# Kernel tuning notes

Hardware: AMD Instinct MI355X
Metric: run time of the kernel (lower is better)

## Reference

```python
import jax, jax.numpy as jnp
import numpy as np

B, S, QD, KD, AD, H = 64, 2048, 1024, 512, 512, 8
NEG = -1e10  # masked_fill value from original code
SCALING = 1.0  # default forward arg


def setup_inputs() -> dict:
    key = jax.random.key(0)
    ks = jax.random.split(key, 6)
    query = jax.random.normal(ks[0], (B, QD), dtype=jnp.float32)
    keys = jax.random.normal(ks[1], (B, S, KD), dtype=jnp.float32)
    value = jax.random.normal(ks[2], (B, S, KD), dtype=jnp.float32)
    key_len = jax.random.randint(ks[3], (B,), 1, S + 1, dtype=jnp.int32)
    Wq = jax.random.normal(ks[4], (H, AD, QD), dtype=jnp.float32) * 0.02
    Wk = jax.random.normal(ks[5], (H, AD, KD), dtype=jnp.float32) * 0.02
    return {"query": query, "keys": keys, "value": value, "key_len": key_len,
            "Wq": Wq, "Wk": Wk}


def reference(query, keys, value, key_len, Wq, Wk):
    # per-head query projection: (B, H, AD)
    q = jnp.einsum('bq,haq->bha', query, Wq)
    # per-head key projection: (B, H, S, AD)
    k = jnp.einsum('bsk,hak->bhsa', keys, Wk)
    # single-step dot attention energies: (B, H, S)
    energy = jnp.einsum('bha,bhsa->bhs', q, k)
    # padding mask: positions >= key_len are masked
    mask = jnp.arange(keys.shape[1])[None, None, :] >= key_len[:, None, None]
    energy = jnp.where(mask, NEG, energy)
    attn = jax.nn.softmax(energy * SCALING, axis=-1)  # (B, H, S)
    # per-head contexts: (B, H, KD), concatenated over heads -> (B, H*KD)
    context = jnp.einsum('bhs,bsd->bhd', attn, value)
    contexts = context.reshape(context.shape[0], -1)
    return contexts, attn
```

## Files before the change

### kernel.cpp

```cpp
#include <hip/hip_runtime.h>
#include <math.h>


#define B_  64
#define S_  2048
#define QD_ 1024
#define KD_ 512
#define AD_ 512
#define H_  8

__global__ __launch_bounds__(256) void k1_qproj(const float* __restrict__ query,
                                                const float* __restrict__ Wq,
                                                float* __restrict__ qo) {
    __shared__ float As[16][65];
    __shared__ float Ws[64][65];
    const int t = threadIdx.x;
    const int m0 = blockIdx.x * 16, n0 = blockIdx.y * 64;
    const int nl = t & 63, mb = (t >> 6) * 4;
    float acc[4] = {0.f, 0.f, 0.f, 0.f};
    for (int kc = 0; kc < QD_; kc += 64) {
#pragma unroll
        for (int i = 0; i < 4; ++i) {
            int idx = t + i * 256, r = idx >> 6, c = idx & 63;
            As[r][c] = query[(m0 + r) * QD_ + kc + c];
        }
#pragma unroll
        for (int i = 0; i < 16; ++i) {
            int idx = t + i * 256, r = idx >> 6, c = idx & 63;
            Ws[r][c] = Wq[(size_t)(n0 + r) * QD_ + kc + c];
        }
        __syncthreads();
#pragma unroll
        for (int k = 0; k < 64; ++k) {
            float w = Ws[nl][k];
#pragma unroll
            for (int j = 0; j < 4; ++j) acc[j] += As[mb + j][k] * w;
        }
        __syncthreads();
    }
#pragma unroll
    for (int j = 0; j < 4; ++j)
        qo[(m0 + mb + j) * (H_ * AD_) + n0 + nl] = acc[j];
}

__global__ __launch_bounds__(256) void k2_qk(const float* __restrict__ q,
                                             const float* __restrict__ Wk,
                                             float* __restrict__ qk) {
    __shared__ float As[16][65];
    __shared__ float Ws[64][65];
    const int t = threadIdx.x;
    const int m0 = blockIdx.x * 16, n0 = blockIdx.y * 64, h = blockIdx.z;
    const float* Wh = Wk + (size_t)h * AD_ * KD_;
    const int nl = t & 63, mb = (t >> 6) * 4;
    float acc[4] = {0.f, 0.f, 0.f, 0.f};
    for (int ac = 0; ac < AD_; ac += 64) {
#pragma unroll
        for (int i = 0; i < 4; ++i) {
            int idx = t + i * 256, r = idx >> 6, c = idx & 63;
            As[r][c] = q[(m0 + r) * (H_ * AD_) + h * AD_ + ac + c];
        }
#pragma unroll
        for (int i = 0; i < 16; ++i) {
            int idx = t + i * 256, r = idx >> 6, c = idx & 63;
            Ws[r][c] = Wh[(size_t)(ac + r) * KD_ + n0 + c];
        }
        __syncthreads();
#pragma unroll
        for (int k = 0; k < 64; ++k) {
            float w = Ws[k][nl];
#pragma unroll
            for (int j = 0; j < 4; ++j) acc[j] += As[mb + j][k] * w;
        }
        __syncthreads();
    }
#pragma unroll
    for (int j = 0; j < 4; ++j)
        qk[(m0 + mb + j) * (H_ * KD_) + h * KD_ + n0 + nl] = acc[j];
}

__global__ __launch_bounds__(256) void k3_energy(const float* __restrict__ keys,
                                                 const float* __restrict__ qk,
                                                 const int* __restrict__ key_len,
                                                 float* __restrict__ energy) {
    const int b = blockIdx.y;
    const int klen = key_len[b];
    const int s0 = blockIdx.x * 128;
    if (s0 >= klen) return;
    const int t = threadIdx.x;
    const int lane = t & 63, w = t >> 6;

    const float4* qk4 = reinterpret_cast<const float4*>(qk + (size_t)b * (H_ * KD_));
    float qkr[8][8];
#pragma unroll
    for (int h = 0; h < H_; ++h) {
        float4 u0 = qk4[h * (KD_ / 4) + lane * 2];
        float4 u1 = qk4[h * (KD_ / 4) + lane * 2 + 1];
        qkr[h][0] = u0.x; qkr[h][1] = u0.y; qkr[h][2] = u0.z; qkr[h][3] = u0.w;
        qkr[h][4] = u1.x; qkr[h][5] = u1.y; qkr[h][6] = u1.z; qkr[h][7] = u1.w;
    }

    const int sbeg = s0 + w * 32;
    for (int i = 0; i < 32; ++i) {
        int s = sbeg + i;
        if (s >= klen) break;
        const float4* kp = reinterpret_cast<const float4*>(
            keys + (size_t)(b * S_ + s) * KD_ + lane * 8);
        float4 k0 = kp[0], k1 = kp[1];
        float kf[8] = {k0.x, k0.y, k0.z, k0.w, k1.x, k1.y, k1.z, k1.w};
        float partial[8];
#pragma unroll
        for (int h = 0; h < H_; ++h) {
            float p = 0.f;
#pragma unroll
            for (int j = 0; j < 8; ++j) p += kf[j] * qkr[h][j];
            partial[h] = p;
        }
#pragma unroll
        for (int h = 0; h < H_; ++h) {
#pragma unroll
            for (int off = 32; off >= 1; off >>= 1)
                partial[h] += __shfl_xor(partial[h], off, 64);
        }
#pragma unroll
        for (int h = 0; h < H_; ++h)
            if (lane == h) energy[((size_t)b * H_ + h) * S_ + s] = partial[h];
    }
}

__global__ __launch_bounds__(256) void k4_softmax(const float* __restrict__ energy,
                                                  const int* __restrict__ key_len,
                                                  float* __restrict__ attn,
                                                  float* __restrict__ ctx_zero) {
    const int bh = blockIdx.x;
    const int b = bh >> 3;
    const int t = threadIdx.x;
    ctx_zero[bh * 512 + t] = 0.f;
    ctx_zero[bh * 512 + 256 + t] = 0.f;

    const int klen = key_len[b];
    const float* e = energy + (size_t)bh * S_;
    float ev[8];
    float m = -3.0e38f;
#pragma unroll
    for (int j = 0; j < 8; ++j) {
        int s = t + j * 256;
        float x = (s < klen) ? e[s] : -3.0e38f;
        ev[j] = x;
        m = fmaxf(m, x);
    }
#pragma unroll
    for (int off = 32; off >= 1; off >>= 1) m = fmaxf(m, __shfl_xor(m, off, 64));
    __shared__ float redm[4];
    if ((t & 63) == 0) redm[t >> 6] = m;
    __syncthreads();
    m = fmaxf(fmaxf(redm[0], redm[1]), fmaxf(redm[2], redm[3]));

    float sum = 0.f;
#pragma unroll
    for (int j = 0; j < 8; ++j) {
        int s = t + j * 256;
        float p = (s < klen) ? __expf(ev[j] - m) : 0.f;
        ev[j] = p;
        sum += p;
    }
#pragma unroll
    for (int off = 32; off >= 1; off >>= 1) sum += __shfl_xor(sum, off, 64);
    __shared__ float reds[4];
    if ((t & 63) == 0) reds[t >> 6] = sum;
    __syncthreads();
    sum = reds[0] + reds[1] + reds[2] + reds[3];
    const float inv = 1.f / sum;

    float* a = attn + (size_t)bh * S_;
#pragma unroll
    for (int j = 0; j < 8; ++j) a[t + j * 256] = ev[j] * inv;
}

__global__ __launch_bounds__(256) void k5_context(const float* __restrict__ value,
                                                  const float* __restrict__ attn,
                                                  const int* __restrict__ key_len,
                                                  float* __restrict__ ctx) {
    const int b = blockIdx.y;
    const int klen = key_len[b];
    const int s_base = blockIdx.x * 128;
    if (s_base >= klen) return;
    const int t = threadIdx.x;

    __shared__ float at[8][128];
#pragma unroll
    for (int i = 0; i < 4; ++i) {
        int idx = t + i * 256, h = idx >> 7, si = idx & 127;
        int s = s_base + si;
        at[h][si] = (s < klen) ? attn[((size_t)b * H_ + h) * S_ + s] : 0.f;
    }
    __syncthreads();

    const int tt = t & 127;
    const int sh = t >> 7;
    const int d = tt * 4;
    const int siBeg = sh * 64;
    const int siEnd = min(siBeg + 64, klen - s_base);

    float4 acc[8];
#pragma unroll
    for (int h = 0; h < H_; ++h) acc[h] = make_float4(0.f, 0.f, 0.f, 0.f);

    for (int si = siBeg; si < siEnd; ++si) {
        const float4 v = *reinterpret_cast<const float4*>(
            value + (size_t)(b * S_ + s_base + si) * KD_ + d);
#pragma unroll
        for (int h = 0; h < H_; ++h) {
            float a = at[h][si];
            acc[h].x += a * v.x; acc[h].y += a * v.y;
            acc[h].z += a * v.z; acc[h].w += a * v.w;
        }
    }

    float* cb = ctx + (size_t)b * (H_ * KD_);
#pragma unroll
    for (int h = 0; h < H_; ++h) {
        atomicAdd(&cb[h * KD_ + d + 0], acc[h].x);
        atomicAdd(&cb[h * KD_ + d + 1], acc[h].y);
        atomicAdd(&cb[h * KD_ + d + 2], acc[h].z);
        atomicAdd(&cb[h * KD_ + d + 3], acc[h].w);
    }
}

extern "C" void kernel_launch(void* const* d_in, const int* in_sizes, int n_in,
                              void* d_out, int out_size, void* d_ws, size_t ws_size,
                              hipStream_t stream) {
    const float* query   = (const float*)d_in[0];
    const float* keys    = (const float*)d_in[1];
    const float* value   = (const float*)d_in[2];
    const int*   key_len = (const int*)d_in[3];
    const float* Wq      = (const float*)d_in[4];
    const float* Wk      = (const float*)d_in[5];

    float* out = (float*)d_out;
    float* ctx_out  = out;
    float* attn_out = out + (size_t)B_ * H_ * KD_;

    float* ws    = (float*)d_ws;
    float* q_ws  = ws;
    float* qk_ws = ws + (size_t)B_ * H_ * AD_;
    float* e_ws  = qk_ws + (size_t)B_ * H_ * KD_;

    hipLaunchKernelGGL(k1_qproj, dim3(4, 64), dim3(256), 0, stream, query, Wq, q_ws);
    hipLaunchKernelGGL(k2_qk, dim3(4, 8, 8), dim3(256), 0, stream, q_ws, Wk, qk_ws);
    hipLaunchKernelGGL(k3_energy, dim3(16, 64), dim3(256), 0, stream,
                       keys, qk_ws, key_len, e_ws);
    hipLaunchKernelGGL(k4_softmax, dim3(512), dim3(256), 0, stream,
                       e_ws, key_len, attn_out, ctx_out);
    hipLaunchKernelGGL(k5_context, dim3(16, 64), dim3(256), 0, stream,
                       value, attn_out, key_len, ctx_out);
}
```

Before: 645.2 us.

## Halve energy block size, use transpose-style shuffle reduction, replace context atomics with partial reduce

```diff
diff --git a/kernel.cpp b/kernel.cpp
--- a/kernel.cpp
+++ b/kernel.cpp
@@ -84,7 +84,7 @@
                                                  float* __restrict__ energy) {
     const int b = blockIdx.y;
     const int klen = key_len[b];
-    const int s0 = blockIdx.x * 128;
+    const int s0 = blockIdx.x * 64;
     if (s0 >= klen) return;
     const int t = threadIdx.x;
     const int lane = t & 63, w = t >> 6;
@@ -99,43 +99,63 @@
         qkr[h][4] = u1.x; qkr[h][5] = u1.y; qkr[h][6] = u1.z; qkr[h][7] = u1.w;
     }
 
-    const int sbeg = s0 + w * 32;
-    for (int i = 0; i < 32; ++i) {
-        int s = sbeg + i;
-        if (s >= klen) break;
+    const int sbeg = s0 + w * 16;
+    const int count = min(16, klen - sbeg);
+    if (count <= 0) return;
+
+    auto row = [&](int s) {
         const float4* kp = reinterpret_cast<const float4*>(
             keys + (size_t)(b * S_ + s) * KD_ + lane * 8);
         float4 k0 = kp[0], k1 = kp[1];
         float kf[8] = {k0.x, k0.y, k0.z, k0.w, k1.x, k1.y, k1.z, k1.w};
-        float partial[8];
-#pragma unroll
-        for (int h = 0; h < H_; ++h) {
-            float p = 0.f;
-#pragma unroll
-            for (int j = 0; j < 8; ++j) p += kf[j] * qkr[h][j];
-            partial[h] = p;
-        }
-#pragma unroll
-        for (int h = 0; h < H_; ++h) {
-#pragma unroll
-            for (int off = 32; off >= 1; off >>= 1)
-                partial[h] += __shfl_xor(partial[h], off, 64);
-        }
-#pragma unroll
-        for (int h = 0; h < H_; ++h)
-            if (lane == h) energy[((size_t)b * H_ + h) * S_ + s] = partial[h];
+        float p[8];
+#pragma unroll
+        for (int h = 0; h < 8; ++h) {
+            float a = 0.f;
+#pragma unroll
+            for (int j = 0; j < 8; ++j) a += kf[j] * qkr[h][j];
+            p[h] = a;
+        }
+#pragma unroll
+        for (int j = 0; j < 4; ++j) {
+            float keep = (lane & 1) ? p[j + 4] : p[j];
+            float send = (lane & 1) ? p[j] : p[j + 4];
+            p[j] = keep + __shfl_xor(send, 1, 64);
+        }
+#pragma unroll
+        for (int j = 0; j < 2; ++j) {
+            float keep = (lane & 2) ? p[j + 2] : p[j];
+            float send = (lane & 2) ? p[j] : p[j + 2];
+            p[j] = keep + __shfl_xor(send, 2, 64);
+        }
+        {
+            float keep = (lane & 4) ? p[1] : p[0];
+            float send = (lane & 4) ? p[0] : p[1];
+            p[0] = keep + __shfl_xor(send, 4, 64);
+        }
+        p[0] += __shfl_xor(p[0], 8, 64);
+        p[0] += __shfl_xor(p[0], 16, 64);
+        p[0] += __shfl_xor(p[0], 32, 64);
+        if (lane < 8) {
+            const int h = ((lane & 1) << 2) | (lane & 2) | ((lane >> 2) & 1);
+            energy[((size_t)b * H_ + h) * S_ + s] = p[0];
+        }
+    };
+
+    if (count == 16) {
+#pragma unroll 4
+        for (int i = 0; i < 16; ++i) row(sbeg + i);
+    } else {
+        for (int i = 0; i < count; ++i) row(sbeg + i);
     }
 }
 
 __global__ __launch_bounds__(256) void k4_softmax(const float* __restrict__ energy,
                                                   const int* __restrict__ key_len,
-                                                  float* __restrict__ attn,
-                                                  float* __restrict__ ctx_zero) {
+                                                  float* __restrict__ attn) {
     const int bh = blockIdx.x;
     const int b = bh >> 3;
     const int t = threadIdx.x;
-    ctx_zero[bh * 512 + t] = 0.f;
-    ctx_zero[bh * 512 + 256 + t] = 0.f;
 
     const int klen = key_len[b];
     const float* e = energy + (size_t)bh * S_;
@@ -179,7 +199,7 @@
 __global__ __launch_bounds__(256) void k5_context(const float* __restrict__ value,
                                                   const float* __restrict__ attn,
                                                   const int* __restrict__ key_len,
-                                                  float* __restrict__ ctx) {
+                                                  float* __restrict__ part) {
     const int b = blockIdx.y;
     const int klen = key_len[b];
     const int s_base = blockIdx.x * 128;
@@ -195,35 +215,56 @@
     }
     __syncthreads();
 
-    const int tt = t & 127;
+    const int col = t & 127;
     const int sh = t >> 7;
-    const int d = tt * 4;
-    const int siBeg = sh * 64;
-    const int siEnd = min(siBeg + 64, klen - s_base);
+    const int d = col * 4;
+    const int base_si = sh * 64;
+    const int valid = min(64, klen - s_base - base_si);
+    if (valid <= 0) return;
 
     float4 acc[8];
 #pragma unroll
     for (int h = 0; h < H_; ++h) acc[h] = make_float4(0.f, 0.f, 0.f, 0.f);
 
-    for (int si = siBeg; si < siEnd; ++si) {
+    auto step = [&](int si) {
         const float4 v = *reinterpret_cast<const float4*>(
-            value + (size_t)(b * S_ + s_base + si) * KD_ + d);
+            value + (size_t)(b * S_ + s_base + base_si + si) * KD_ + d);
 #pragma unroll
         for (int h = 0; h < H_; ++h) {
-            float a = at[h][si];
+            const float a = at[h][base_si + si];
             acc[h].x += a * v.x; acc[h].y += a * v.y;
             acc[h].z += a * v.z; acc[h].w += a * v.w;
         }
-    }
-
-    float* cb = ctx + (size_t)b * (H_ * KD_);
-#pragma unroll
-    for (int h = 0; h < H_; ++h) {
-        atomicAdd(&cb[h * KD_ + d + 0], acc[h].x);
-        atomicAdd(&cb[h * KD_ + d + 1], acc[h].y);
-        atomicAdd(&cb[h * KD_ + d + 2], acc[h].z);
-        atomicAdd(&cb[h * KD_ + d + 3], acc[h].w);
-    }
+    };
+    if (valid == 64) {
+#pragma unroll 4
+        for (int si = 0; si < 64; ++si) step(si);
+    } else {
+        for (int si = 0; si < valid; ++si) step(si);
+    }
+
+    const int p = blockIdx.x * 2 + sh;
+    float* pp = part + (((size_t)p * B_ + b) * H_) * KD_;
+#pragma unroll
+    for (int h = 0; h < H_; ++h)
+        *reinterpret_cast<float4*>(pp + h * KD_ + d) = acc[h];
+}
+
+__global__ __launch_bounds__(256) void k6_reduce(const float* __restrict__ part,
+                                                 const int* __restrict__ key_len,
+                                                 float* __restrict__ ctx) {
+    const int g = blockIdx.x * 256 + threadIdx.x;
+    const int d4 = g & 127;
+    const int h = (g >> 7) & 7;
+    const int b = g >> 10;
+    const int nc = (key_len[b] + 63) >> 6;
+    float4 s = make_float4(0.f, 0.f, 0.f, 0.f);
+    for (int p = 0; p < nc; ++p) {
+        const float4 v = *reinterpret_cast<const float4*>(
+            part + (((size_t)p * B_ + b) * H_ + h) * KD_ + d4 * 4);
+        s.x += v.x; s.y += v.y; s.z += v.z; s.w += v.w;
+    }
+    *reinterpret_cast<float4*>(ctx + ((size_t)b * H_ + h) * KD_ + d4 * 4) = s;
 }
 
 extern "C" void kernel_launch(void* const* d_in, const int* in_sizes, int n_in,
@@ -240,17 +281,20 @@
     float* ctx_out  = out;
     float* attn_out = out + (size_t)B_ * H_ * KD_;
 
-    float* ws    = (float*)d_ws;
-    float* q_ws  = ws;
-    float* qk_ws = ws + (size_t)B_ * H_ * AD_;
-    float* e_ws  = qk_ws + (size_t)B_ * H_ * KD_;
+    float* ws      = (float*)d_ws;
+    float* q_ws    = ws;
+    float* qk_ws   = ws + (size_t)B_ * H_ * AD_;
+    float* e_ws    = qk_ws + (size_t)B_ * H_ * KD_;
+    float* part_ws = e_ws + (size_t)B_ * H_ * S_;
 
     hipLaunchKernelGGL(k1_qproj, dim3(4, 64), dim3(256), 0, stream, query, Wq, q_ws);
     hipLaunchKernelGGL(k2_qk, dim3(4, 8, 8), dim3(256), 0, stream, q_ws, Wk, qk_ws);
-    hipLaunchKernelGGL(k3_energy, dim3(16, 64), dim3(256), 0, stream,
+    hipLaunchKernelGGL(k3_energy, dim3(32, 64), dim3(256), 0, stream,
                        keys, qk_ws, key_len, e_ws);
     hipLaunchKernelGGL(k4_softmax, dim3(512), dim3(256), 0, stream,
-                       e_ws, key_len, attn_out, ctx_out);
+                       e_ws, key_len, attn_out);
     hipLaunchKernelGGL(k5_context, dim3(16, 64), dim3(256), 0, stream,
-                       value, attn_out, key_len, ctx_out);
-}
+                       value, attn_out, key_len, part_ws);
+    hipLaunchKernelGGL(k6_reduce, dim3(256), dim3(256), 0, stream,
+                       part_ws, key_len, ctx_out);
+}
```

Result: faster. 585.2 us (-9.3%).
